# Optimization experiments

Measured on AMD Instinct MI355X. Metric: run time of the kernel, lower is better.

The kernel has to match this reference:

```python
import jax, jax.numpy as jnp
import numpy as np

N_AUTHOR = 50000
N_PAPER = 50000
D_IN = 128      # input feature dim == hidden_channels so both layers share weight shapes
HID = 128
OUT = 32
N_LAYERS = 2
N_EDGES = 800000
NEG_SLOPE = 0.01  # F.leaky_relu default


def setup_inputs() -> dict:
    key = jax.random.key(0)
    ks = jax.random.split(key, 10)
    return {
        "x_author": jax.random.normal(ks[0], (N_AUTHOR, D_IN), jnp.float32),
        "x_paper": jax.random.normal(ks[1], (N_PAPER, D_IN), jnp.float32),
        # edge_index[0] = source node ids, edge_index[1] = destination node ids
        "edge_writes": jax.random.randint(ks[2], (2, N_EDGES), 0, N_PAPER, jnp.int32),      # author -> paper
        "edge_written_by": jax.random.randint(ks[3], (2, N_EDGES), 0, N_AUTHOR, jnp.int32),  # paper  -> author
        "edge_cites": jax.random.randint(ks[4], (2, N_EDGES), 0, N_PAPER, jnp.int32),        # paper  -> paper
        # SAGEConv params, stacked [layer, relation, in, out]; relation order:
        # 0: writes (a->p), 1: written_by (p->a), 2: cites (p->p)
        "Wl": jax.random.normal(ks[5], (N_LAYERS, 3, D_IN, HID), jnp.float32) * 0.05,  # lin_l (messages, has bias)
        "bl": jnp.zeros((N_LAYERS, 3, HID), jnp.float32),
        "Wr": jax.random.normal(ks[6], (N_LAYERS, 3, D_IN, HID), jnp.float32) * 0.05,  # lin_r (root, no bias)
        "lin_W": jax.random.normal(ks[7], (HID, OUT), jnp.float32) * 0.05,
        "lin_b": jnp.zeros((OUT,), jnp.float32),
    }


def _mean_aggr(x_src, edge, n_dst):
    # mean of source features over incoming edges per destination node; 0 for isolated nodes
    src, dst = edge[0], edge[1]
    s = jax.ops.segment_sum(x_src[src], dst, num_segments=n_dst)           # [n_dst, d]
    cnt = jax.ops.segment_sum(jnp.ones((dst.shape[0],), x_src.dtype), dst, num_segments=n_dst)
    return s / jnp.maximum(cnt, 1.0)[:, None]


def _sage(x_src, x_dst, edge, W_l, b_l, W_r):
    # PyG SAGEConv (mean aggr): lin_l(mean_j x_src[j]) + lin_r(x_dst)
    return _mean_aggr(x_src, edge, x_dst.shape[0]) @ W_l + b_l + x_dst @ W_r


def reference(x_author, x_paper, edge_writes, edge_written_by, edge_cites,
              Wl, bl, Wr, lin_W, lin_b):
    a, p = x_author, x_paper
    for l in range(N_LAYERS):
        # HeteroConv default aggr='sum' over edge types sharing a dst node type
        p_new = (_sage(a, p, edge_writes, Wl[l, 0], bl[l, 0], Wr[l, 0])
                 + _sage(p, p, edge_cites, Wl[l, 2], bl[l, 2], Wr[l, 2]))
        a_new = _sage(p, a, edge_written_by, Wl[l, 1], bl[l, 1], Wr[l, 1])
        a = jax.nn.leaky_relu(a_new, NEG_SLOPE)
        p = jax.nn.leaky_relu(p_new, NEG_SLOPE)
    return a @ lin_W + lin_b  # [N_AUTHOR, OUT]
```

## Files before the change

### kernel.cpp

```cpp
#include <hip/hip_runtime.h>

#define NA 50000
#define NP 50000
#define NE 800000
#define D 128
#define OUTD 32
#define NSEG 150000
#define DD (D * D)
#define NCH 196
#define NBK 588
#define CHE 4096
#define CAP2 4608
#define ZROW 50000

typedef float f32x4 __attribute__((ext_vector_type(4)));
typedef short s16x8 __attribute__((ext_vector_type(8)));

__device__ __forceinline__ ushort f2b(float f) {
    uint x = __float_as_uint(f);
    x += ((x >> 16) & 1u) + 0x7fffu;
    return (ushort)(x >> 16);
}


#define CVT_BLOCKS 12500
#define PREP_BLOCKS 466
#define SCAT_BLOCKS NBK

__global__ __launch_bounds__(256) void front2(
    const float* __restrict__ xa, const float* __restrict__ xp,
    ushort* __restrict__ oa, ushort* __restrict__ op,
    const float* __restrict__ Wl, const float* __restrict__ Wr,
    const float* __restrict__ linW, const float* __restrict__ bl,
    ushort* __restrict__ wt, float* __restrict__ bsum_p,
    ushort* __restrict__ p1b,
    const int* __restrict__ sw, const int* __restrict__ dw,
    const int* __restrict__ sc_, const int* __restrict__ dc,
    const int* __restrict__ swb, const int* __restrict__ dwb,
    int* __restrict__ cursor, uint* __restrict__ bucketed)
{
    __shared__ uint recbuf[CHE];
    __shared__ int hist[NCH], gbase[NCH], cnt2[NCH];
    int b = blockIdx.x, t = threadIdx.x;
    if (b < CVT_BLOCKS) {
        int i = b * 256 + t;
        const int per = NA * D / 4;
        const float* src; ushort* dst; int li;
        if (i < per) { src = xa; dst = oa; li = i; }
        else { src = xp; dst = op; li = i - per; }
        float4 v = *(const float4*)&src[(size_t)li * 4];
        ushort4 o;
        o.x = f2b(v.x); o.y = f2b(v.y); o.z = f2b(v.z); o.w = f2b(v.w);
        *(ushort4*)&dst[(size_t)li * 4] = o;
    } else if (b < CVT_BLOCKS + PREP_BLOCKS) {
        int b2 = b - CVT_BLOCKS;
        if (b2 < 448) {
            int job = b2 >> 6;
            int idx = (b2 & 63) * 256 + t;
            int n = idx >> 7, k = idx & 127;
            const float* src;
            float add = 0.f;
            switch (job) {
                case 0: src = Wl + 0 * DD; break;
                case 1: src = Wl + 2 * DD; break;
                case 2: src = Wr + 0 * DD; add = Wr[2 * DD + k * D + n]; break;
                case 3: src = Wl + 1 * DD; break;
                case 4: src = Wr + 1 * DD; break;
                case 5: src = Wl + 4 * DD; break;
                default: src = Wr + 4 * DD; break;
            }
            wt[(size_t)job * DD + idx] = f2b(src[k * D + n] + add);
        } else if (b2 < 464) {
            int idx = (b2 - 448) * 256 + t;
            int n = idx >> 7, k = idx & 127;
            wt[(size_t)7 * DD + idx] = f2b(linW[k * OUTD + n]);
        } else if (b2 == 464) {
            if (t < D) bsum_p[t] = bl[t] + bl[2 * D + t];
        } else {
            if (t < 64)       ((uint*)(oa + (size_t)ZROW * D))[t] = 0;
            else if (t < 128) ((uint*)(op + (size_t)ZROW * D))[t - 64] = 0;
            else if (t < 192) ((uint*)(p1b + (size_t)ZROW * D))[t - 128] = 0;
        }
    } else {
        int hb = b - CVT_BLOCKS - PREP_BLOCKS;
        int r = hb / NCH, c = hb % NCH;
        const int* sp = (r == 0) ? sw : ((r == 1) ? sc_ : swb);
        const int* dp = (r == 0) ? dw : ((r == 1) ? dc : dwb);
        for (int i = t; i < NCH; i += 256) { hist[i] = 0; cnt2[i] = 0; }
        __syncthreads();
        int base = c * CHE;
#pragma unroll
        for (int i = 0; i < 16; ++i) {
            int e = base + i * 256 + t;
            uint rec = 0xFFFFFFFFu;
            if (e < NE) {
                int d = dp[e], s = sp[e];
                rec = ((uint)d << 16) | (uint)s;
                atomicAdd(&hist[d >> 8], 1);
            }
            recbuf[i * 256 + t] = rec;
        }
        __syncthreads();
        for (int i = t; i < NCH; i += 256)
            gbase[i] = (r * NCH + i) * CAP2 + atomicAdd(&cursor[r * NCH + i], hist[i]);
        __syncthreads();
#pragma unroll
        for (int i = 0; i < 16; ++i) {
            uint rec = recbuf[i * 256 + t];
            if (rec != 0xFFFFFFFFu) {
                int dg = rec >> 24;
                int rk = atomicAdd(&cnt2[dg], 1);
                bucketed[gbase[dg] + rk] = rec;
            }
        }
    }
}


__global__ __launch_bounds__(1024) void bucket_sort2(
    const uint* __restrict__ bucketed, const int* __restrict__ cursor,
    ushort* __restrict__ csr16, int2* __restrict__ meta)
{
    __shared__ int h[256], bb[256], c3[256];
    int gd = blockIdx.x, t = threadIdx.x;
    int r = gd / NCH, hb = gd % NCH;
    int beg = gd * CAP2;
    int n = cursor[gd];
    if (t < 256) { h[t] = 0; c3[t] = 0; }
    __syncthreads();
    for (int i = t; i < n; i += 1024)
        atomicAdd(&h[(bucketed[beg + i] >> 16) & 255], 1);
    __syncthreads();
    if (t < 64) {
        int carry = 0;
#pragma unroll
        for (int rnd = 0; rnd < 4; ++rnd) {
            int idx = rnd * 64 + t;
            int v = h[idx], x = v;
#pragma unroll
            for (int off = 1; off < 64; off <<= 1) {
                int y = __shfl_up(x, off, 64);
                if (t >= off) x += y;
            }
            bb[idx] = carry + x - v;
            carry += __shfl(x, 63, 64);
        }
    }
    __syncthreads();
    if (t < 256) {
        int dst = hb * 256 + t;
        if (dst < 50000) meta[r * 50000 + dst] = make_int2(beg + bb[t], h[t]);
    }
    for (int i = t; i < n; i += 1024) {
        uint rec = bucketed[beg + i];
        int low = (rec >> 16) & 255;
        int rk = atomicAdd(&c3[low], 1);
        csr16[beg + bb[low] + rk] = (ushort)(rec & 0xffffu);
    }
}


#define DOT2(a, u, m) asm("v_dot2_f32_bf16 %0, %1, %2, %0" : "+v"(a) : "v"(u), "v"(m))

__device__ __forceinline__ void gather_node(
    const ushort* __restrict__ x, const ushort* __restrict__ bk, int n,
    int l, int g, int c, ushort* __restrict__ outp)
{
    float acc[8];
#pragma unroll
    for (int k = 0; k < 8; ++k) acc[k] = 0.f;
    const uint mlo = 0x00003f80u;
    const uint mhi = 0x3f800000u;
    const uint cb = (uint)c * 16;

    for (int base = 0; base < n; base += 64) {
        int rem = n - base;
        int m = rem > 64 ? 64 : rem;
        int idx = (l < m) ? (int)bk[base + l] : ZROW;
        int mceil = (m + 3) & ~3;
#pragma unroll 4
        for (int j = 0; j < mceil; j += 4) {
            int row = __shfl(idx, j + g, 64);
            uint4 u = *(const uint4*)((const char*)x + (((uint)row << 8) + cb));
            DOT2(acc[0], u.x, mlo); DOT2(acc[1], u.x, mhi);
            DOT2(acc[2], u.y, mlo); DOT2(acc[3], u.y, mhi);
            DOT2(acc[4], u.z, mlo); DOT2(acc[5], u.z, mhi);
            DOT2(acc[6], u.w, mlo); DOT2(acc[7], u.w, mhi);
        }
    }
#pragma unroll
    for (int k = 0; k < 8; ++k) {
        acc[k] += __shfl_xor(acc[k], 16, 64);
        acc[k] += __shfl_xor(acc[k], 32, 64);
    }
    if (g == 0) {
        float scl = (n > 0) ? 1.0f / (float)n : 0.f;
        uint4 o;
        o.x = (uint)f2b(acc[0] * scl) | ((uint)f2b(acc[1] * scl) << 16);
        o.y = (uint)f2b(acc[2] * scl) | ((uint)f2b(acc[3] * scl) << 16);
        o.z = (uint)f2b(acc[4] * scl) | ((uint)f2b(acc[5] * scl) << 16);
        o.w = (uint)f2b(acc[6] * scl) | ((uint)f2b(acc[7] * scl) << 16);
        *(uint4*)&outp[c * 8] = o;
    }
}

__global__ __launch_bounds__(256) void gather3(
    const ushort* __restrict__ xa, const ushort* __restrict__ xp,
    const int2* __restrict__ meta, const ushort* __restrict__ csr16,
    ushort* __restrict__ agg3)
{
    int wid = (blockIdx.x * 256 + threadIdx.x) >> 6;
    if (wid >= NSEG) return;
    const ushort* x = (wid < 50000) ? xa : xp;
    int l = threadIdx.x & 63;
    int2 m = meta[wid];
    int beg = __builtin_amdgcn_readfirstlane(m.x);
    int n = __builtin_amdgcn_readfirstlane(m.y);
    gather_node(x, csr16 + beg, n, l, l >> 4, l & 15,
                agg3 + (size_t)wid * D);
}

__global__ __launch_bounds__(256) void gather_l1(
    const ushort* __restrict__ x, const int2* __restrict__ meta,
    const ushort* __restrict__ csr16, ushort* __restrict__ out)
{
    int wid = (blockIdx.x * 256 + threadIdx.x) >> 6;
    if (wid >= NA) return;
    int l = threadIdx.x & 63;
    int2 m = meta[100000 + wid];
    int beg = __builtin_amdgcn_readfirstlane(m.x);
    int n = __builtin_amdgcn_readfirstlane(m.y);
    gather_node(x, csr16 + beg, n, l, l >> 4, l & 15,
                out + (size_t)wid * D);
}


#define LDA 136

__device__ __forceinline__ void gemm_core(
    ushort* As, f32x4 (&acc)[2][4],
    const ushort* __restrict__ A0, const ushort* __restrict__ WT0,
    const ushort* __restrict__ A1, const ushort* __restrict__ WT1,
    const ushort* __restrict__ A2, const ushort* __restrict__ WT2,
    int nseg, int brow, int M)
{
    const int t = threadIdx.x;
    const int w = t >> 6;
    const int l = t & 63;
    const int wr = w >> 1, wc = w & 1;
    const int l15 = l & 15, l4 = l >> 4;

    for (int s = 0; s < nseg; ++s) {
        const ushort* A = (s == 0) ? A0 : ((s == 1) ? A1 : A2);
        const ushort* WT = (s == 0) ? WT0 : ((s == 1) ? WT1 : WT2);

        if (s) __syncthreads();
#pragma unroll
        for (int it = 0; it < 4; ++it) {
            int f = it * 256 + t;
            int row = f >> 4, cc = f & 15;
            int grow = brow + row;
            float4 v = make_float4(0.f, 0.f, 0.f, 0.f);
            if (grow < M) v = *(const float4*)&A[(size_t)grow * D + cc * 8];
            *(float4*)&As[row * LDA + cc * 8] = v;
        }
        s16x8 Bf[4][4];
#pragma unroll
        for (int ni = 0; ni < 4; ++ni)
#pragma unroll
            for (int ks = 0; ks < 4; ++ks)
                Bf[ni][ks] = *(const s16x8*)&WT[(size_t)(wc * 64 + ni * 16 + l15) * D + ks * 32 + l4 * 8];
        __syncthreads();

#pragma unroll
        for (int ks = 0; ks < 4; ++ks) {
            s16x8 af[2];
#pragma unroll
            for (int mi = 0; mi < 2; ++mi)
                af[mi] = *(const s16x8*)&As[(wr * 32 + mi * 16 + l15) * LDA + ks * 32 + l4 * 8];
#pragma unroll
            for (int mi = 0; mi < 2; ++mi)
#pragma unroll
                for (int ni = 0; ni < 4; ++ni)
                    acc[mi][ni] = __builtin_amdgcn_mfma_f32_16x16x32_bf16(
                        af[mi], Bf[ni][ks], acc[mi][ni], 0, 0, 0);
        }
    }
}

__global__ __launch_bounds__(256) void gemm_pair(
    const ushort* __restrict__ agg3, const ushort* __restrict__ xb_p,
    const ushort* __restrict__ xb_a, const ushort* __restrict__ wt,
    const float* __restrict__ bsum_p, const float* __restrict__ bl,
    ushort* __restrict__ p1b, ushort* __restrict__ a1b)
{
    __shared__ ushort As[64 * LDA];
    const int t = threadIdx.x;
    const int w = t >> 6;
    const int l = t & 63;
    const int wr = w >> 1, wc = w & 1;
    const int l15 = l & 15, l4 = l >> 4;

    f32x4 acc[2][4];
#pragma unroll
    for (int i = 0; i < 2; ++i)
#pragma unroll
        for (int j = 0; j < 4; ++j) acc[i][j] = (f32x4){0.f, 0.f, 0.f, 0.f};

    bool isP = blockIdx.x < 782;
    int bIdx = isP ? blockIdx.x : blockIdx.x - 782;
    int brow = bIdx * 64;
    const float* bias;
    ushort* C;
    if (isP) {
        gemm_core(As, acc, agg3, wt + 0 * DD, agg3 + (size_t)50000 * D, wt + 1 * DD,
                  xb_p, wt + 2 * DD, 3, brow, NP);
        bias = bsum_p; C = p1b;
    } else {
        gemm_core(As, acc, agg3 + (size_t)100000 * D, wt + 3 * DD, xb_a, wt + 4 * DD,
                  nullptr, nullptr, 2, brow, NA);
        bias = bl + 1 * D; C = a1b;
    }

#pragma unroll
    for (int mi = 0; mi < 2; ++mi) {
#pragma unroll
        for (int ni = 0; ni < 4; ++ni) {
            int col = wc * 64 + ni * 16 + l15;
            float bb = bias[col];
#pragma unroll
            for (int r = 0; r < 4; ++r) {
                int grow = brow + wr * 32 + mi * 16 + l4 * 4 + r;
                if (grow >= 50000) continue;
                float v = acc[mi][ni][r] + bb;
                v = v > 0.f ? v : 0.01f * v;
                C[(size_t)grow * D + col] = f2b(v);
            }
        }
    }
}

__global__ __launch_bounds__(256) void gemm_final(
    const ushort* __restrict__ A0, const ushort* __restrict__ WT0,
    const ushort* __restrict__ A1, const ushort* __restrict__ WT1,
    const float* __restrict__ bias,
    const ushort* __restrict__ linWT, const float* __restrict__ linb,
    float* __restrict__ fout, int M)
{
    __shared__ ushort As[64 * LDA];
    const int t = threadIdx.x;
    const int w = t >> 6;
    const int l = t & 63;
    const int wr = w >> 1, wc = w & 1;
    const int l15 = l & 15, l4 = l >> 4;
    const int brow = blockIdx.x * 64;

    f32x4 acc[2][4];
#pragma unroll
    for (int i = 0; i < 2; ++i)
#pragma unroll
        for (int j = 0; j < 4; ++j) acc[i][j] = (f32x4){0.f, 0.f, 0.f, 0.f};

    gemm_core(As, acc, A0, WT0, A1, WT1, nullptr, nullptr, 2, brow, M);

    __syncthreads();
#pragma unroll
    for (int mi = 0; mi < 2; ++mi) {
#pragma unroll
        for (int ni = 0; ni < 4; ++ni) {
            int col = wc * 64 + ni * 16 + l15;
            float bb = bias[col];
#pragma unroll
            for (int r = 0; r < 4; ++r) {
                int row = wr * 32 + mi * 16 + l4 * 4 + r;
                float v = acc[mi][ni][r] + bb;
                v = v > 0.f ? v : 0.01f * v;
                As[row * LDA + col] = f2b(v);
            }
        }
    }
    __syncthreads();
    f32x4 a2c[2];
    a2c[0] = (f32x4){0.f, 0.f, 0.f, 0.f};
    a2c[1] = (f32x4){0.f, 0.f, 0.f, 0.f};
#pragma unroll
    for (int ks = 0; ks < 4; ++ks) {
        s16x8 af = *(const s16x8*)&As[(w * 16 + l15) * LDA + ks * 32 + l4 * 8];
#pragma unroll
        for (int ni = 0; ni < 2; ++ni) {
            s16x8 bf = *(const s16x8*)&linWT[(size_t)(ni * 16 + l15) * D + ks * 32 + l4 * 8];
            a2c[ni] = __builtin_amdgcn_mfma_f32_16x16x32_bf16(af, bf, a2c[ni], 0, 0, 0);
        }
    }
#pragma unroll
    for (int ni = 0; ni < 2; ++ni) {
        int col = ni * 16 + l15;
        float bb = linb[col];
#pragma unroll
        for (int r = 0; r < 4; ++r) {
            int grow = brow + w * 16 + l4 * 4 + r;
            if (grow < M) fout[(size_t)grow * OUTD + col] = a2c[ni][r] + bb;
        }
    }
}


extern "C" void kernel_launch(void* const* d_in, const int* in_sizes, int n_in,
                              void* d_out, int out_size, void* d_ws, size_t ws_size,
                              hipStream_t stream)
{
    const float* x_author = (const float*)d_in[0];
    const float* x_paper  = (const float*)d_in[1];
    const int*   e_w      = (const int*)d_in[2];
    const int*   e_wb     = (const int*)d_in[3];
    const int*   e_c      = (const int*)d_in[4];
    const float* Wl       = (const float*)d_in[5];
    const float* bl       = (const float*)d_in[6];
    const float* Wr       = (const float*)d_in[7];
    const float* linW     = (const float*)d_in[8];
    const float* linb     = (const float*)d_in[9];
    float* out = (float*)d_out;

    int* ib = (int*)d_ws;
    int* cursor  = ib;
    int2* meta   = (int2*)(ib + 640);
    uint* bucketed = (uint*)(ib + 300672);
    ushort* csr16  = (ushort*)(ib + 3010176);
    float* bsum_p  = (float*)(ib + 4364928);
    ushort* ub = (ushort*)(ib + 4365056);
    const size_t R1 = 50001 * (size_t)D;
    ushort* wt   = ub;
    ushort* xb_a = ub + 131072;
    ushort* xb_p = xb_a + R1;
    ushort* agg3 = xb_p + R1;
    ushort* p1b  = agg3 + (size_t)NSEG * D;
    ushort* a1b  = p1b + R1;
    ushort* g2b  = agg3;

    hipMemsetAsync(cursor, 0, NBK * sizeof(int), stream);

    front2<<<CVT_BLOCKS + PREP_BLOCKS + SCAT_BLOCKS, 256, 0, stream>>>(
        x_author, x_paper, xb_a, xb_p,
        Wl, Wr, linW, bl, wt, bsum_p, p1b,
        e_w, e_w + NE, e_c, e_c + NE, e_wb, e_wb + NE,
        cursor, bucketed);

    bucket_sort2<<<NBK, 1024, 0, stream>>>(bucketed, cursor, csr16, meta);

    gather3<<<NSEG * 64 / 256, 256, 0, stream>>>(xb_a, xb_p, meta, csr16, agg3);

    gemm_pair<<<1564, 256, 0, stream>>>(agg3, xb_p, xb_a, wt, bsum_p, bl, p1b, a1b);

    gather_l1<<<NA * 64 / 256, 256, 0, stream>>>(p1b, meta, csr16, g2b);

    gemm_final<<<(NA + 63) / 64, 256, 0, stream>>>(
        g2b, wt + 5 * DD, a1b, wt + 6 * DD, bl + 4 * D, wt + 7 * DD, linb, out, NA);
}
```

Baseline: 246.0 us.

## Stage bucket scatter in LDS so global writes become coalesced

The edge-bucketing pass now counts first, prefix-sums the coarse bucket histogram, and scatters records into a locally sorted shared-memory buffer. It then writes that buffer to global memory contiguously, replacing the random per-record global stores. The fine sort in bucket_sort2 likewise stages the 16-bit indices in shared memory and copies them out as 32-bit words. The cost is re-reading the edge arrays in a second pass, extra barriers, and more shared memory per block.

```diff
diff --git a/kernel.cpp b/kernel.cpp
--- a/kernel.cpp
+++ b/kernel.cpp
@@ -39,8 +39,9 @@
     const int* __restrict__ swb, const int* __restrict__ dwb,
     int* __restrict__ cursor, uint* __restrict__ bucketed)
 {
-    __shared__ uint recbuf[CHE];
-    __shared__ int hist[NCH], gbase[NCH], cnt2[NCH];
+    __shared__ uint srt[CHE];
+    __shared__ int hist[NCH], lb[NCH], goff[NCH], cnt2[NCH];
+    __shared__ int tot;
     int b = blockIdx.x, t = threadIdx.x;
     if (b < CVT_BLOCKS) {
         int i = b * 256 + t;
@@ -92,26 +93,48 @@
 #pragma unroll
         for (int i = 0; i < 16; ++i) {
             int e = base + i * 256 + t;
-            uint rec = 0xFFFFFFFFu;
+            if (e < NE) atomicAdd(&hist[dp[e] >> 8], 1);
+        }
+        __syncthreads();
+        if (t < 64) {
+            int carry = 0;
+#pragma unroll
+            for (int rnd = 0; rnd < 4; ++rnd) {
+                int idx = rnd * 64 + t;
+                int v = (idx < NCH) ? hist[idx] : 0;
+                int x = v;
+#pragma unroll
+                for (int off = 1; off < 64; off <<= 1) {
+                    int y = __shfl_up(x, off, 64);
+                    if (t >= off) x += y;
+                }
+                if (idx < NCH) lb[idx] = carry + x - v;
+                carry += __shfl(x, 63, 64);
+            }
+            if (t == 0) tot = carry;
+        }
+        __syncthreads();
+        for (int i = t; i < NCH; i += 256) {
+            int gd = r * NCH + i;
+            int g0 = gd * CAP2 + atomicAdd(&cursor[gd], hist[i]);
+            goff[i] = g0 - lb[i];
+        }
+        __syncthreads();
+#pragma unroll
+        for (int i = 0; i < 16; ++i) {
+            int e = base + i * 256 + t;
             if (e < NE) {
-                int d = dp[e], s = sp[e];
-                rec = ((uint)d << 16) | (uint)s;
-                atomicAdd(&hist[d >> 8], 1);
-            }
-            recbuf[i * 256 + t] = rec;
-        }
-        __syncthreads();
-        for (int i = t; i < NCH; i += 256)
-            gbase[i] = (r * NCH + i) * CAP2 + atomicAdd(&cursor[r * NCH + i], hist[i]);
-        __syncthreads();
-#pragma unroll
-        for (int i = 0; i < 16; ++i) {
-            uint rec = recbuf[i * 256 + t];
-            if (rec != 0xFFFFFFFFu) {
+                uint rec = ((uint)dp[e] << 16) | (uint)sp[e];
                 int dg = rec >> 24;
                 int rk = atomicAdd(&cnt2[dg], 1);
-                bucketed[gbase[dg] + rk] = rec;
-            }
+                srt[lb[dg] + rk] = rec;
+            }
+        }
+        __syncthreads();
+        int T = tot;
+        for (int i = t; i < T; i += 256) {
+            uint rec = srt[i];
+            bucketed[goff[rec >> 24] + i] = rec;
         }
     }
 }
@@ -122,6 +145,7 @@
     ushort* __restrict__ csr16, int2* __restrict__ meta)
 {
     __shared__ int h[256], bb[256], c3[256];
+    __shared__ ushort srt16[CAP2];
     int gd = blockIdx.x, t = threadIdx.x;
     int r = gd / NCH, hb = gd % NCH;
     int beg = gd * CAP2;
@@ -155,8 +179,14 @@
         uint rec = bucketed[beg + i];
         int low = (rec >> 16) & 255;
         int rk = atomicAdd(&c3[low], 1);
-        csr16[beg + bb[low] + rk] = (ushort)(rec & 0xffffu);
-    }
+        srt16[bb[low] + rk] = (ushort)(rec & 0xffffu);
+    }
+    __syncthreads();
+    int nu = (n + 1) >> 1;
+    uint* dst32 = (uint*)(csr16 + beg);
+    const uint* src32 = (const uint*)srt16;
+    for (int i = t; i < nu; i += 1024)
+        dst32[i] = src32[i];
 }
 
 
```

Result: faster. 232.9 us (-5.3%).
